# Kernel tuning notes

Hardware: AMD Instinct MI355X
Metric: run time of the kernel (lower is better)

## Reference

```python
import jax, jax.numpy as jnp
import numpy as np

B, T, C_IN, DIM, NFFT, HOP = 8, 1024, 256, 512, 1024, 256
NOUT = NFFT // 2 + 1
BB_DIL = (1, 1, 2, 2, 4, 4, 8, 8)
RES_DIL = (1, 3, 5)
N_RES = 3


def conv1d(x, w, b, dilation=1, groups=1, padding=0):
    # x: (B,C,T), w: (O, I/groups, K)
    y = jax.lax.conv_general_dilated(
        x, w, window_strides=(1,), padding=[(padding, padding)],
        rhs_dilation=(dilation,), dimension_numbers=('NCH', 'OIH', 'NCH'),
        feature_group_count=groups)
    return y + b[None, :, None]


def layernorm(x, g, b, eps=1e-6):
    m = jnp.mean(x, -1, keepdims=True)
    v = jnp.mean((x - m) ** 2, -1, keepdims=True)
    return (x - m) * jax.lax.rsqrt(v + eps) * g + b


def istft(spec, window):
    # spec: (B, F, Tf) complex, center=True, hann window, win_length=n_fft
    Bsz, F_, Tf = spec.shape
    frames = jnp.fft.irfft(spec, n=NFFT, axis=1)            # (B, n_fft, Tf)
    frames = jnp.transpose(frames, (0, 2, 1)) * window       # (B, Tf, n_fft)
    L = NFFT + HOP * (Tf - 1)
    idx = jnp.arange(Tf)[:, None] * HOP + jnp.arange(NFFT)[None, :]  # (Tf, n_fft)
    y = jnp.zeros((Bsz, L), frames.dtype).at[:, idx].add(frames)
    env = jnp.zeros((L,), window.dtype).at[idx].add(
        jnp.broadcast_to(window ** 2, (Tf, NFFT)))
    y = y / jnp.where(env > 1e-11, env, 1.0)
    start = NFFT // 2
    return y[:, start:start + HOP * (Tf - 1)]


def setup_inputs() -> dict:
    key = jax.random.key(0)
    ks = iter(jax.random.split(key, 64))
    r = lambda *s: jax.random.normal(next(ks), s, jnp.float32) * 0.02
    return {
        'x': jax.random.normal(next(ks), (B, T, C_IN), jnp.float32),
        'conv_in_w': r(DIM, C_IN, 7), 'conv_in_b': r(DIM),
        'skip_w': r(DIM, C_IN, 1), 'skip_b': r(DIM),
        'bb_dw_w': r(8, DIM, 1, 7), 'bb_dw_b': r(8, DIM),
        'bb_ln_g': jnp.ones((8, DIM), jnp.float32), 'bb_ln_b': jnp.zeros((8, DIM), jnp.float32),
        'bb_pw1_w': r(8, 4 * DIM, DIM), 'bb_pw1_b': r(8, 4 * DIM),
        'bb_pw2_w': r(8, DIM, 4 * DIM), 'bb_pw2_b': r(8, DIM),
        'bb_gamma': jnp.full((8, DIM), 1e-6, jnp.float32),
        'res_w1': r(N_RES, 3, DIM, DIM, 3), 'res_b1': r(N_RES, 3, DIM),
        'res_w2': r(N_RES, 3, DIM, DIM, 3), 'res_b2': r(N_RES, 3, DIM),
        'ln_g': jnp.ones((DIM,), jnp.float32), 'ln_b': jnp.zeros((DIM,), jnp.float32),
        'mag_w1': r(DIM, DIM), 'mag_b1': r(DIM),
        'mag_w2': r(NOUT, DIM), 'mag_b2': r(NOUT),
        'ph_w': r(NOUT, DIM), 'ph_b': r(NOUT),
        'cumsum_w': jnp.linspace(0.05, 0.4, NOUT, dtype=jnp.float32)[None, :],
        'window': (0.5 - 0.5 * jnp.cos(2.0 * jnp.pi * jnp.arange(NFFT) / NFFT)).astype(jnp.float32),
    }


def reference(x, conv_in_w, conv_in_b, skip_w, skip_b,
              bb_dw_w, bb_dw_b, bb_ln_g, bb_ln_b,
              bb_pw1_w, bb_pw1_b, bb_pw2_w, bb_pw2_b, bb_gamma,
              res_w1, res_b1, res_w2, res_b2,
              ln_g, ln_b, mag_w1, mag_b1, mag_w2, mag_b2,
              ph_w, ph_b, cumsum_w, window):
    # (B,T,C) -> (B,C,T)
    h = jnp.transpose(x, (0, 2, 1))
    skip = conv1d(h, skip_w, skip_b)                     # (B,DIM,T)
    hp = jnp.pad(h, ((0, 0), (0, 0), (3, 3)), mode='reflect')
    h = conv1d(hp, conv_in_w, conv_in_b)                 # kernel 7, pad 0 -> (B,DIM,T)
    # ConvNeXt backbone
    for i, d in enumerate(BB_DIL):
        res = h
        pad = (7 + (d - 1) * 6) // 2
        y = conv1d(h, bb_dw_w[i], bb_dw_b[i], dilation=d, groups=DIM, padding=pad)
        y = jnp.transpose(y, (0, 2, 1))                  # (B,T,DIM)
        y = layernorm(y, bb_ln_g[i], bb_ln_b[i])
        y = jax.nn.gelu(y @ bb_pw1_w[i].T + bb_pw1_b[i], approximate=False)
        y = y @ bb_pw2_w[i].T + bb_pw2_b[i]
        y = bb_gamma[i] * y
        h = res + jnp.transpose(y, (0, 2, 1))
    h = h + skip                                         # same length T
    # Residual dilated conv stacks
    for i in range(N_RES):
        for j, d in enumerate(RES_DIL):
            y = conv1d(h, res_w1[i, j], res_b1[i, j], dilation=d, padding=d)
            y = jax.nn.leaky_relu(y, 0.1)
            y = conv1d(y, res_w2[i, j], res_b2[i, j], padding=1)
            h = h + y
    h = jnp.transpose(h, (0, 2, 1))                      # (B,T,DIM)
    h = layernorm(h, ln_g, ln_b)
    # magnitude head
    m = jax.nn.gelu(h @ mag_w1.T + mag_b1, approximate=False)
    log_mag = m @ mag_w2.T + mag_b2
    mag = jnp.exp(jnp.clip(log_mag, -10.0, 10.0))        # (B,T,NOUT)
    # instantaneous-frequency phase head
    inst = jnp.tanh(h @ ph_w.T + ph_b) * jnp.pi
    phase = jnp.cumsum(inst * cumsum_w, axis=1)
    phase = jnp.remainder(phase + jnp.pi, 2.0 * jnp.pi) - jnp.pi
    # synthesize
    spec = jax.lax.complex(mag * jnp.cos(phase), mag * jnp.sin(phase))
    spec = jnp.transpose(spec, (0, 2, 1))                # (B,F,T)
    return istft(spec, window)
```

## Files before the change

kernel.cpp:

```cpp
#include <hip/hip_runtime.h>
#include <math.h>

constexpr int Bv = 8, Tv = 1024, DIMC = 512, NOUTC = 513;
constexpr int Mrows = Bv * Tv;
constexpr int LDS_S = 1056;
constexpr float PI_F = 3.14159265358979323846f;
constexpr float TWOPI_F = 6.28318530717958647692f;

struct TapInfo { int n; int off[7]; };
struct PtrTable { _Float16* h[36]; };

enum { BND_NONE = 0, BND_ZERO, BND_REFLECT };

typedef _Float16 half8v __attribute__((ext_vector_type(8)));
typedef float f32x4 __attribute__((ext_vector_type(4)));

__device__ __forceinline__ void gld_lds16(const void* g, void* l) {
  __builtin_amdgcn_global_load_lds(
      (const __attribute__((address_space(1))) unsigned int*)g,
      (__attribute__((address_space(3))) unsigned int*)l, 16, 0, 0);
}

enum { MEPI_GELU_H = 0, MEPI_GAMMARES };

template<int EPI, int TN>
__global__ __launch_bounds__(256)
void mfma_gemm(const _Float16* __restrict__ A, int lda,
               const _Float16* __restrict__ W, int K,
               const float* __restrict__ bias,
               const float* __restrict__ aux,
               float* __restrict__ hio,
               _Float16* __restrict__ Ch,
               int N, int ldc)
{
  constexpr int NFR = TN / 32;
  __shared__ _Float16 sA[2][128 * 32];
  __shared__ _Float16 sB[2][TN * 32];
  const int m0 = blockIdx.x * 128;
  const int n0 = blockIdx.y * TN;
  const int tid = threadIdx.x;
  const int wid = tid >> 6, lane = tid & 63;
  const int wr = wid >> 1, wc = wid & 1;
  const int fr = lane & 15, fq = lane >> 4;

  f32x4 acc[4][NFR] = {};

  const int rbase = tid >> 2;
  const int kwithin = (tid & 3) * 8;
  const int nkc = K >> 5;
  const int aBase = (wr * 64 + fr) * 32 + fq * 8;
  const int bBase = (wc * (TN / 2) + fr) * 32 + fq * 8;

  const _Float16* arow[2];
  #pragma unroll
  for (int s = 0; s < 2; ++s)
    arow[s] = A + (size_t)(m0 + s * 64 + rbase) * lda + kwithin;

  auto STAGE = [&](int kc, int buf) {
    const int k0 = kc << 5;
    #pragma unroll
    for (int s = 0; s < 2; ++s)
      gld_lds16(arow[s] + k0, (char*)&sA[buf][0] + s * 4096 + wid * 1024);
    #pragma unroll
    for (int s = 0; s < TN / 64; ++s) {
      size_t bo = (size_t)(n0 + s * 64 + rbase) * K + kwithin + k0;
      gld_lds16(W + bo, (char*)&sB[buf][0] + s * 4096 + wid * 1024);
    }
  };
  auto COMPUTE = [&](int buf) {
    half8v aF[4], bF[NFR];
    #pragma unroll
    for (int i = 0; i < 4; ++i) aF[i] = *(const half8v*)&sA[buf][aBase + i * 512];
    #pragma unroll
    for (int j = 0; j < NFR; ++j) bF[j] = *(const half8v*)&sB[buf][bBase + j * 512];
    #pragma unroll
    for (int i = 0; i < 4; ++i)
      #pragma unroll
      for (int j = 0; j < NFR; ++j)
        acc[i][j] = __builtin_amdgcn_mfma_f32_16x16x32_f16(aF[i], bF[j], acc[i][j], 0, 0, 0);
  };

  STAGE(0, 0);
  __syncthreads();
  int cur = 0;
  for (int kc = 0; kc < nkc; ++kc) {
    if (kc + 1 < nkc) STAGE(kc + 1, cur ^ 1);
    COMPUTE(cur);
    __syncthreads();
    cur ^= 1;
  }

  #pragma unroll
  for (int j = 0; j < NFR; ++j) {
    const int n = n0 + wc * (TN / 2) + j * 16 + fr;
    const float bj = bias[n];
    const float gj = (EPI == MEPI_GAMMARES) ? aux[n] : 0.f;
    #pragma unroll
    for (int i = 0; i < 4; ++i) {
      const int mB = m0 + wr * 64 + i * 16 + fq * 4;
      #pragma unroll
      for (int r = 0; r < 4; ++r) {
        const int m = mB + r;
        float v = acc[i][j][r] + bj;
        if (EPI == MEPI_GELU_H) {
          v = 0.5f * v * (1.f + erff(v * 0.70710678118654752f));
          Ch[(size_t)m * ldc + n] = (_Float16)v;
        } else {
          hio[(size_t)m * ldc + n] += gj * v;
        }
      }
    }
  }
}

enum { SEPI_F32 = 0, SEPI_LEAKY_SPLIT, SEPI_ADDRES_SPLIT,
       SEPI_GELU_SPLIT, SEPI_EXPCLIP, SEPI_TANHCW };

template<int EPI, int BND, int TN>
__global__ __launch_bounds__(256)
void mfma_gemm_split(const _Float16* __restrict__ Ah, const _Float16* __restrict__ Al, int lda,
                     const _Float16* __restrict__ Wh, const _Float16* __restrict__ Wl, int K,
                     const float* __restrict__ bias,
                     const float* __restrict__ aux,
                     float* __restrict__ hio,
                     float* __restrict__ Cf,
                     _Float16* __restrict__ Chh, _Float16* __restrict__ Chl,
                     int N, int ldc,
                     const _Float16* __restrict__ zpage,
                     TapInfo taps)
{
  constexpr int NFR = TN / 32;
  __shared__ _Float16 sAh[2][128 * 32];
  __shared__ _Float16 sAl[2][128 * 32];
  __shared__ _Float16 sBh[2][TN * 32];
  __shared__ _Float16 sBl[2][TN * 32];
  const int m0 = blockIdx.x * 128;
  const int n0 = blockIdx.y * TN;
  const int tid = threadIdx.x;
  const int wid = tid >> 6, lane = tid & 63;
  const int wr = wid >> 1, wc = wid & 1;
  const int fr = lane & 15, fq = lane >> 4;

  f32x4 acc[4][NFR] = {};

  const int t0 = m0 & (Tv - 1);
  const int rbase = tid >> 2;
  const int kwithin = (tid & 3) * 8;
  const int nkc = K >> 5;
  const int NT = taps.n * nkc;
  const int aBase = (wr * 64 + fr) * 32 + fq * 8;
  const int bBase = (wc * (TN / 2) + fr) * 32 + fq * 8;

  auto STAGE = [&](int st, int buf) {
    int tap = (taps.n == 1) ? 0 : (st / nkc);
    int kc = st - tap * nkc;
    const int k0 = kc << 5;
    const int off = (BND == BND_NONE) ? 0 : taps.off[tap];
    const _Float16* Wth = Wh + (size_t)tap * N * K;
    const _Float16* Wtl = Wl + (size_t)tap * N * K;
    #pragma unroll
    for (int s = 0; s < 2; ++s) {
      int t = t0 + s * 64 + rbase + off;
      bool valid = true;
      if (BND == BND_REFLECT) t = (t < 0) ? -t : (t >= Tv ? 2 * Tv - 2 - t : t);
      else if (BND == BND_ZERO) valid = (t >= 0) && (t < Tv);
      size_t ro = (size_t)(m0 - t0 + t) * lda + kwithin + k0;
      const void* sh = valid ? (const void*)(Ah + ro) : (const void*)zpage;
      const void* sl = valid ? (const void*)(Al + ro) : (const void*)zpage;
      gld_lds16(sh, (char*)&sAh[buf][0] + s * 4096 + wid * 1024);
      gld_lds16(sl, (char*)&sAl[buf][0] + s * 4096 + wid * 1024);
    }
    #pragma unroll
    for (int s = 0; s < TN / 64; ++s) {
      size_t bo = (size_t)(n0 + s * 64 + rbase) * K + kwithin + k0;
      gld_lds16(Wth + bo, (char*)&sBh[buf][0] + s * 4096 + wid * 1024);
      gld_lds16(Wtl + bo, (char*)&sBl[buf][0] + s * 4096 + wid * 1024);
    }
  };

  auto COMPUTE = [&](int buf) {
    half8v ah[4], al[4], bh[NFR], bl[NFR];
    #pragma unroll
    for (int i = 0; i < 4; ++i) {
      ah[i] = *(const half8v*)&sAh[buf][aBase + i * 512];
      al[i] = *(const half8v*)&sAl[buf][aBase + i * 512];
    }
    #pragma unroll
    for (int j = 0; j < NFR; ++j) {
      bh[j] = *(const half8v*)&sBh[buf][bBase + j * 512];
      bl[j] = *(const half8v*)&sBl[buf][bBase + j * 512];
    }
    #pragma unroll
    for (int i = 0; i < 4; ++i)
      #pragma unroll
      for (int j = 0; j < NFR; ++j) {
        acc[i][j] = __builtin_amdgcn_mfma_f32_16x16x32_f16(ah[i], bh[j], acc[i][j], 0, 0, 0);
        acc[i][j] = __builtin_amdgcn_mfma_f32_16x16x32_f16(ah[i], bl[j], acc[i][j], 0, 0, 0);
        acc[i][j] = __builtin_amdgcn_mfma_f32_16x16x32_f16(al[i], bh[j], acc[i][j], 0, 0, 0);
      }
  };

  STAGE(0, 0);
  __syncthreads();
  int cur = 0;
  for (int st = 0; st < NT; ++st) {
    if (st + 1 < NT) STAGE(st + 1, cur ^ 1);
    COMPUTE(cur);
    __syncthreads();
    cur ^= 1;
  }

  #pragma unroll
  for (int j = 0; j < NFR; ++j) {
    const int n = n0 + wc * (TN / 2) + j * 16 + fr;
    const bool nok = (n < N);
    const float bj = (nok && bias) ? bias[n] : 0.f;
    const float ax = (EPI == SEPI_TANHCW && nok) ? aux[n] : 0.f;
    #pragma unroll
    for (int i = 0; i < 4; ++i) {
      const int mB = m0 + wr * 64 + i * 16 + fq * 4;
      #pragma unroll
      for (int r = 0; r < 4; ++r) {
        const int m = mB + r;
        float v = acc[i][j][r] + bj;
        if (!nok) continue;
        if (EPI == SEPI_F32) {
          Cf[(size_t)m * ldc + n] = v;
        } else if (EPI == SEPI_GELU_SPLIT) {
          v = 0.5f * v * (1.f + erff(v * 0.70710678118654752f));
          _Float16 hi = (_Float16)v;
          Chh[(size_t)m * ldc + n] = hi;
          Chl[(size_t)m * ldc + n] = (_Float16)(v - (float)hi);
        } else if (EPI == SEPI_EXPCLIP) {
          Cf[(size_t)m * ldc + n] = expf(fminf(fmaxf(v, -10.f), 10.f));
        } else if (EPI == SEPI_TANHCW) {
          Cf[(size_t)m * ldc + n] = tanhf(v) * PI_F * ax;
        }
      }
    }
  }
}

enum { REPI_LEAKY = 0, REPI_ADDRES };

template<int EPI>
__global__ __launch_bounds__(256)
void res_gemm(const _Float16* __restrict__ Ah, const _Float16* __restrict__ Al,
              const _Float16* __restrict__ Wh, const _Float16* __restrict__ Wl,
              const float* __restrict__ bias,
              float* __restrict__ hio,
              _Float16* __restrict__ Chh, _Float16* __restrict__ Chl,
              const _Float16* __restrict__ zpage,
              int d)
{
  __shared__ _Float16 sAh_[160 * 32];
  __shared__ _Float16 sAl_[160 * 32];
  __shared__ _Float16 sB_[3 * 2 * 64 * 32];
  const int m0 = blockIdx.x * 128;
  const int n0 = blockIdx.y * 64;
  const int tid = threadIdx.x;
  const int wid = tid >> 6, lane = tid & 63;
  const int wr = wid >> 1, wc = wid & 1;
  const int fr = lane & 15, fq = lane >> 4;
  const int t0 = m0 & (Tv - 1);

  f32x4 acc[4][2] = {};
  const int offs[3] = {-d, 0, d};

  for (int kc = 0; kc < 16; ++kc) {
    const int k0h = kc << 5;
    #pragma unroll
    for (int it = 0; it < 5; ++it) {
      int cb = it * 4 + wid;
      int half = (cb >= 10) ? 1 : 0;
      int rb = (cb - half * 10) * 16;
      int row = rb + (lane >> 2);
      int slot_g = (lane & 3) ^ ((row >> 1) & 3);
      int t = t0 - 16 + row;
      bool valid = (t >= 0) && (t < Tv);
      const _Float16* srcb = half ? Al : Ah;
      const void* src = valid
          ? (const void*)(srcb + (size_t)(m0 - t0 + t) * DIMC + k0h + slot_g * 8)
          : (const void*)(zpage + slot_g * 8);
      void* dst = (char*)(half ? sAl_ : sAh_) + rb * 64;
      gld_lds16(src, dst);
    }
    #pragma unroll
    for (int it = 0; it < 6; ++it) {
      int cb = it * 4 + wid;
      int tap = cb >> 3;
      int r2 = cb & 7;
      int half = r2 >> 2;
      int rb = (r2 & 3) * 16;
      int row = rb + (lane >> 2);
      int slot_g = (lane & 3) ^ ((row >> 1) & 3);
      const _Float16* srcb = (half ? Wl : Wh) + (size_t)tap * 512 * 512
                           + (size_t)(n0 + row) * 512 + k0h + slot_g * 8;
      void* dst = (char*)sB_ + ((size_t)(tap * 2 + half) * 64 + rb) * 64;
      gld_lds16(srcb, dst);
    }
    __syncthreads();

    #pragma unroll
    for (int tap = 0; tap < 3; ++tap) {
      const int off = offs[tap];
      half8v ah[4], al[4], bh[2], bl[2];
      #pragma unroll
      for (int i = 0; i < 4; ++i) {
        int rA = wr * 64 + i * 16 + fr + off + 16;
        int ab = rA * 64 + ((fq ^ ((rA >> 1) & 3)) * 16);
        ah[i] = *(const half8v*)((const char*)sAh_ + ab);
        al[i] = *(const half8v*)((const char*)sAl_ + ab);
      }
      #pragma unroll
      for (int j = 0; j < 2; ++j) {
        int rB = wc * 32 + j * 16 + fr;
        int bb = rB * 64 + ((fq ^ ((rB >> 1) & 3)) * 16);
        bh[j] = *(const half8v*)((const char*)sB_ + (tap * 2 + 0) * 4096 + bb);
        bl[j] = *(const half8v*)((const char*)sB_ + (tap * 2 + 1) * 4096 + bb);
      }
      #pragma unroll
      for (int i = 0; i < 4; ++i)
        #pragma unroll
        for (int j = 0; j < 2; ++j) {
          acc[i][j] = __builtin_amdgcn_mfma_f32_16x16x32_f16(ah[i], bh[j], acc[i][j], 0, 0, 0);
          acc[i][j] = __builtin_amdgcn_mfma_f32_16x16x32_f16(ah[i], bl[j], acc[i][j], 0, 0, 0);
          acc[i][j] = __builtin_amdgcn_mfma_f32_16x16x32_f16(al[i], bh[j], acc[i][j], 0, 0, 0);
        }
    }
    __syncthreads();
  }

  #pragma unroll
  for (int j = 0; j < 2; ++j) {
    const int n = n0 + wc * 32 + j * 16 + fr;
    const float bj = bias[n];
    #pragma unroll
    for (int i = 0; i < 4; ++i) {
      const int mB = m0 + wr * 64 + i * 16 + fq * 4;
      #pragma unroll
      for (int r = 0; r < 4; ++r) {
        const int m = mB + r;
        float v = acc[i][j][r] + bj;
        if (EPI == REPI_LEAKY) {
          v = (v > 0.f) ? v : 0.1f * v;
          _Float16 hi = (_Float16)v;
          Chh[(size_t)m * DIMC + n] = hi;
          Chl[(size_t)m * DIMC + n] = (_Float16)(v - (float)hi);
        } else {
          float nh = hio[(size_t)m * DIMC + n] + v;
          hio[(size_t)m * DIMC + n] = nh;
          _Float16 hi = (_Float16)nh;
          Chh[(size_t)m * DIMC + n] = hi;
          Chl[(size_t)m * DIMC + n] = (_Float16)(nh - (float)hi);
        }
      }
    }
  }
}

__global__ __launch_bounds__(256)
void dwln(const float* __restrict__ h, const float* __restrict__ w,
          const float* __restrict__ bias, const float* __restrict__ g,
          const float* __restrict__ be, _Float16* __restrict__ out, int d)
{
  int wid = threadIdx.x >> 6, lane = threadIdx.x & 63;
  int m = (blockIdx.x << 2) + wid;
  int t = m & (Tv - 1);
  int bT = m - t;
  float acc[8];
  #pragma unroll
  for (int q = 0; q < 8; ++q) {
    int c = lane + (q << 6);
    float s = bias[c];
    #pragma unroll
    for (int k = 0; k < 7; ++k) {
      int tt = t + (k - 3) * d;
      if (tt >= 0 && tt < Tv) s = fmaf(h[(size_t)(bT + tt) * DIMC + c], w[c * 7 + k], s);
    }
    acc[q] = s;
  }
  float sum = 0.f;
  #pragma unroll
  for (int q = 0; q < 8; ++q) sum += acc[q];
  #pragma unroll
  for (int o = 32; o > 0; o >>= 1) sum += __shfl_xor(sum, o);
  float mean = sum * (1.f / 512.f);
  float vs = 0.f;
  #pragma unroll
  for (int q = 0; q < 8; ++q) { float dd = acc[q] - mean; vs = fmaf(dd, dd, vs); }
  #pragma unroll
  for (int o = 32; o > 0; o >>= 1) vs += __shfl_xor(vs, o);
  float rstd = rsqrtf(vs * (1.f / 512.f) + 1e-6f);
  #pragma unroll
  for (int q = 0; q < 8; ++q) {
    int c = lane + (q << 6);
    out[(size_t)m * DIMC + c] = (_Float16)((acc[q] - mean) * rstd * g[c] + be[c]);
  }
}

__global__ __launch_bounds__(256)
void lnorm_split(const float* __restrict__ in, const float* __restrict__ g,
                 const float* __restrict__ be,
                 _Float16* __restrict__ ohi, _Float16* __restrict__ olo)
{
  int wid = threadIdx.x >> 6, lane = threadIdx.x & 63;
  int m = (blockIdx.x << 2) + wid;
  const float* row = in + (size_t)m * DIMC;
  float acc[8];
  #pragma unroll
  for (int q = 0; q < 8; ++q) acc[q] = row[lane + (q << 6)];
  float sum = 0.f;
  #pragma unroll
  for (int q = 0; q < 8; ++q) sum += acc[q];
  #pragma unroll
  for (int o = 32; o > 0; o >>= 1) sum += __shfl_xor(sum, o);
  float mean = sum * (1.f / 512.f);
  float vs = 0.f;
  #pragma unroll
  for (int q = 0; q < 8; ++q) { float dd = acc[q] - mean; vs = fmaf(dd, dd, vs); }
  #pragma unroll
  for (int o = 32; o > 0; o >>= 1) vs += __shfl_xor(vs, o);
  float rstd = rsqrtf(vs * (1.f / 512.f) + 1e-6f);
  #pragma unroll
  for (int q = 0; q < 8; ++q) {
    int c = lane + (q << 6);
    float v = (acc[q] - mean) * rstd * g[c] + be[c];
    _Float16 hi = (_Float16)v;
    ohi[(size_t)m * DIMC + c] = hi;
    olo[(size_t)m * DIMC + c] = (_Float16)(v - (float)hi);
  }
}

__global__ __launch_bounds__(256)
void add_split(float* __restrict__ a, const float* __restrict__ b,
               _Float16* __restrict__ hi, _Float16* __restrict__ lo, int n)
{
  int i = blockIdx.x * 256 + threadIdx.x;
  if (i < n) {
    float v = a[i] + b[i]; a[i] = v;
    _Float16 h = (_Float16)v;
    hi[i] = h; lo[i] = (_Float16)(v - (float)h);
  }
}

__global__ __launch_bounds__(256)
void cvt_split(const float* __restrict__ in, _Float16* __restrict__ hi,
               _Float16* __restrict__ lo, int n)
{
  int i = blockIdx.x * 256 + threadIdx.x;
  if (i < n) {
    float v = in[i];
    _Float16 h = (_Float16)v;
    hi[i] = h; lo[i] = (_Float16)(v - (float)h);
  }
}

__global__ __launch_bounds__(256)
void cvt_split_pad(const float* __restrict__ in, _Float16* __restrict__ hi,
                   _Float16* __restrict__ lo, int rows, int cols, int padRows)
{
  int i = blockIdx.x * 256 + threadIdx.x;
  if (i >= padRows * cols) return;
  int r = i / cols;
  float v = (r < rows) ? in[i] : 0.f;
  _Float16 h = (_Float16)v;
  hi[i] = h; lo[i] = (_Float16)(v - (float)h);
}

__global__ __launch_bounds__(256)
void cvt_h(const float* __restrict__ in, _Float16* __restrict__ out, int n)
{
  int i = (blockIdx.x * 256 + threadIdx.x) * 4;
  if (i >= n) return;
  float4 v = *(const float4*)&in[i];
  out[i + 0] = (_Float16)v.x; out[i + 1] = (_Float16)v.y;
  out[i + 2] = (_Float16)v.z; out[i + 3] = (_Float16)v.w;
}

__global__ __launch_bounds__(256)
void repack_split(const float* __restrict__ in, _Float16* __restrict__ hi,
                  _Float16* __restrict__ lo, int O, int C, int KT)
{
  int idx = blockIdx.x * 256 + threadIdx.x;
  if (idx >= O * C) return;
  int o = idx / C, c = idx - o * C;
  for (int k = 0; k < KT; ++k) {
    float v = in[((size_t)o * C + c) * KT + k];
    _Float16 h = (_Float16)v;
    size_t dst = ((size_t)k * O + o) * C + c;
    hi[dst] = h; lo[dst] = (_Float16)(v - (float)h);
  }
}

__global__ __launch_bounds__(256)
void repack_all(const float* __restrict__ res_w1, const float* __restrict__ res_w2,
                PtrTable pt)
{
  int blk = blockIdx.x;
  int conv = blk >> 10;
  int idx = ((blk & 1023) << 8) + threadIdx.x;
  int o = idx >> 9, c = idx & 511;
  const float* src = (conv < 9) ? (res_w1 + (size_t)conv * 786432)
                                : (res_w2 + (size_t)(conv - 9) * 786432);
  _Float16* hi = pt.h[conv * 2];
  _Float16* lo = pt.h[conv * 2 + 1];
  #pragma unroll
  for (int k = 0; k < 3; ++k) {
    float v = src[((size_t)o * 512 + c) * 3 + k];
    _Float16 hh = (_Float16)v;
    size_t dst = ((size_t)k * 512 + o) * 512 + c;
    hi[dst] = hh; lo[dst] = (_Float16)(v - (float)hh);
  }
}

__global__ __launch_bounds__(256)
void zero_fill16(_Float16* __restrict__ p)
{
  int i = threadIdx.x * 8;
  #pragma unroll
  for (int q = 0; q < 8; ++q) p[i + q] = (_Float16)0.f;
}

__global__ __launch_bounds__(256)
void build_basis_split(const float* __restrict__ window,
                       _Float16* __restrict__ bhi, _Float16* __restrict__ blo)
{
  int n = blockIdx.x;
  float wn = window[n];
  const float invN = 1.f / 1024.f;
  for (int j = threadIdx.x; j < LDS_S; j += 256) {
    float coef = 0.f;
    if (j < 513) {
      int k = j;
      if (k == 0)        coef = invN;
      else if (k == 512) coef = (n & 1) ? -invN : invN;
      else {
        int r = (k * n) & 1023;
        coef = 2.f * invN * cosf(TWOPI_F * (float)r * (1.f / 1024.f));
      }
    } else if (j < 1026) {
      int k = j - 513;
      if (k != 0 && k != 512) {
        int r = (k * n) & 1023;
        coef = -2.f * invN * sinf(TWOPI_F * (float)r * (1.f / 1024.f));
      }
    }
    float v = coef * wn;
    _Float16 hi = (_Float16)v;
    bhi[(size_t)n * LDS_S + j] = hi;
    blo[(size_t)n * LDS_S + j] = (_Float16)(v - (float)hi);
  }
}

__global__ __launch_bounds__(256)
void scan_part(const float* __restrict__ dph, float* __restrict__ psum)
{
  int b = blockIdx.x, fg = blockIdx.y;
  int w = threadIdx.x >> 6, lane = threadIdx.x & 63;
  int tc = blockIdx.z * 4 + w;
  int f = fg * 64 + lane;
  if (f >= NOUTC) return;
  const float* p = dph + (size_t)(b * Tv + tc * 32) * NOUTC + f;
  float s = 0.f;
  #pragma unroll 8
  for (int j = 0; j < 32; ++j) s += p[(size_t)j * NOUTC];
  psum[((size_t)b * 32 + tc) * 520 + f] = s;
}

__global__ __launch_bounds__(256)
void scan_off(float* __restrict__ psum)
{
  int idx = blockIdx.x * 256 + threadIdx.x;
  if (idx >= 8 * NOUTC) return;
  int b = idx / NOUTC, f = idx - b * NOUTC;
  float run = 0.f;
  for (int tc = 0; tc < 32; ++tc) {
    size_t o = ((size_t)b * 32 + tc) * 520 + f;
    float v = psum[o];
    psum[o] = run;
    run += v;
  }
}

__global__ __launch_bounds__(256)
void scan_emit(const float* __restrict__ dph, const float* __restrict__ mag,
               const float* __restrict__ psum,
               _Float16* __restrict__ Shi, _Float16* __restrict__ Slo)
{
  int b = blockIdx.x, fg = blockIdx.y;
  int w = threadIdx.x >> 6, lane = threadIdx.x & 63;
  int tc = blockIdx.z * 4 + w;
  int f = fg * 64 + lane;
  if (f >= NOUTC) return;
  float run = psum[((size_t)b * 32 + tc) * 520 + f];
  const size_t base = (size_t)(b * Tv + tc * 32) * NOUTC + f;
  for (int j = 0; j < 32; ++j) {
    run += dph[base + (size_t)j * NOUTC];
    float r = fmodf(run + PI_F, TWOPI_F);
    if (r < 0.f) r += TWOPI_F;
    float wph = r - PI_F;
    float mg = mag[base + (size_t)j * NOUTC];
    float sn, cs;
    sincosf(wph, &sn, &cs);
    size_t mrow = (size_t)(b * Tv + tc * 32 + j) * LDS_S;
    float vc = mg * cs, vs2 = mg * sn;
    _Float16 hc = (_Float16)vc, hs = (_Float16)vs2;
    Shi[mrow + f] = hc;        Slo[mrow + f] = (_Float16)(vc - (float)hc);
    Shi[mrow + 513 + f] = hs;  Slo[mrow + 513 + f] = (_Float16)(vs2 - (float)hs);
  }
}

__global__ __launch_bounds__(256)
void pad_S(_Float16* __restrict__ Shi, _Float16* __restrict__ Slo)
{
  int idx = blockIdx.x * 256 + threadIdx.x;
  if (idx >= Mrows * 30) return;
  int m = idx / 30, c = 1026 + idx % 30;
  Shi[(size_t)m * LDS_S + c] = (_Float16)0.f;
  Slo[(size_t)m * LDS_S + c] = (_Float16)0.f;
}

__global__ __launch_bounds__(256)
void ola(const float* __restrict__ frames, const float* __restrict__ window,
         float* __restrict__ out)
{
  int idx = blockIdx.x * 256 + threadIdx.x;
  if (idx >= Bv * 261888) return;
  int b = idx / 261888;
  int i = idx - b * 261888;
  int l = i + 512;
  int tmax = l >> 8; if (tmax > 1023) tmax = 1023;
  int tmin = (l >= 1023) ? ((l - 1023 + 255) >> 8) : 0;
  float acc = 0.f, env = 0.f;
  for (int t = tmin; t <= tmax; ++t) {
    int n = l - (t << 8);
    acc += frames[(size_t)(b * Tv + t) * 1024 + n];
    float wv = window[n];
    env = fmaf(wv, wv, env);
  }
  out[idx] = acc / (env > 1e-11f ? env : 1.f);
}

extern "C" void kernel_launch(void* const* d_in, const int* in_sizes, int n_in,
                              void* d_out, int out_size, void* d_ws, size_t ws_size,
                              hipStream_t stream)
{
  const float* x         = (const float*)d_in[0];
  const float* conv_in_w = (const float*)d_in[1];
  const float* conv_in_b = (const float*)d_in[2];
  const float* skip_w    = (const float*)d_in[3];
  const float* skip_b    = (const float*)d_in[4];
  const float* bb_dw_w   = (const float*)d_in[5];
  const float* bb_dw_b   = (const float*)d_in[6];
  const float* bb_ln_g   = (const float*)d_in[7];
  const float* bb_ln_b   = (const float*)d_in[8];
  const float* bb_pw1_w  = (const float*)d_in[9];
  const float* bb_pw1_b  = (const float*)d_in[10];
  const float* bb_pw2_w  = (const float*)d_in[11];
  const float* bb_pw2_b  = (const float*)d_in[12];
  const float* bb_gamma  = (const float*)d_in[13];
  const float* res_w1    = (const float*)d_in[14];
  const float* res_b1    = (const float*)d_in[15];
  const float* res_w2    = (const float*)d_in[16];
  const float* res_b2    = (const float*)d_in[17];
  const float* ln_g      = (const float*)d_in[18];
  const float* ln_b      = (const float*)d_in[19];
  const float* mag_w1    = (const float*)d_in[20];
  const float* mag_b1    = (const float*)d_in[21];
  const float* mag_w2    = (const float*)d_in[22];
  const float* mag_b2    = (const float*)d_in[23];
  const float* ph_w      = (const float*)d_in[24];
  const float* ph_b      = (const float*)d_in[25];
  const float* cumsum_w  = (const float*)d_in[26];
  const float* window    = (const float*)d_in[27];
  float* out = (float*)d_out;
  float* ws  = (float*)d_ws;

  float* w_h     = ws;
  float* w_skip  = ws + 4194304;
  float* w_t4    = ws + 8388608;
  float* w_mag   = ws + 12582912;
  float* w_dph   = ws + 16785408;
  float* w_basis = ws + 20987904;
  float* w_big   = ws + 22069248;
  _Float16* t3h  = (_Float16*)w_big;
  _Float16* h_hi = (_Float16*)w_big;
  _Float16* h_lo = h_hi + 4194304;
  _Float16* y_hi = h_hi + 8388608;
  _Float16* y_lo = h_hi + 12582912;
  _Float16* Shi  = (_Float16*)w_big;
  _Float16* Slo  = Shi + 8650752;
  float* w_frames= w_h;

  _Float16* t2h  = (_Float16*)(ws + 30720000);
  _Float16* x_hi = (_Float16*)(ws + 32817152);
  _Float16* x_lo = (_Float16*)(ws + 33865728);
  _Float16* wA_hi= (_Float16*)(ws + 34914304);
  _Float16* wA_lo= (_Float16*)(ws + 35438592);
  _Float16* wB_hi= (_Float16*)(ws + 35962880);
  _Float16* wB_lo= (_Float16*)(ws + 36487168);
  _Float16* zpg  = (_Float16*)(ws + 37011456);
  float* w_psum  = ws + 37012480;

  _Float16* wpw1h = (_Float16*)w_t4;
  _Float16* wpw2h = (_Float16*)w_mag;

  static const size_t slotOffF[18] = {
    8388608, 9175040, 9961472, 10747904, 11534336,
    12582912, 13369344, 14155776, 14942208, 15728640,
    16785408, 17571840, 18358272, 19144704, 19931136,
    32817152, 33603584,
    30720000
  };
  PtrTable pt;
  for (int cv = 0; cv < 18; ++cv) {
    _Float16* hi = (_Float16*)(ws + slotOffF[cv]);
    pt.h[cv * 2] = hi;
    pt.h[cv * 2 + 1] = hi + 786432;
  }

  _Float16* lshi = (_Float16*)w_skip;
  _Float16* lslo = lshi + 4194304;
  _Float16* t4hi = (_Float16*)w_t4;
  _Float16* t4lo = t4hi + 4194304;
  _Float16* m1hi = t2h;
  _Float16* m1lo = t2h + 262144;
  _Float16* m2hi = t2h + 524288;
  _Float16* m2lo = t2h + 851968;
  _Float16* phhi = t2h + 1179648;
  _Float16* phlo = t2h + 1507328;
  _Float16* bhi  = (_Float16*)w_basis;
  _Float16* blo  = bhi + 1081344;

  dim3 blk(256);
  TapInfo tp1{1, {0}};

  zero_fill16<<<dim3(1), blk, 0, stream>>>(zpg);
  cvt_split<<<dim3(8192 * 256 / 256), blk, 0, stream>>>(x, x_hi, x_lo, 8192 * 256);
  cvt_h<<<dim3(8388608 / 4 / 256), blk, 0, stream>>>(bb_pw1_w, wpw1h, 8388608);
  cvt_h<<<dim3(8388608 / 4 / 256), blk, 0, stream>>>(bb_pw2_w, wpw2h, 8388608);

  repack_split<<<dim3(512 * 256 / 256), blk, 0, stream>>>(conv_in_w, wA_hi, wA_lo, 512, 256, 7);
  {
    TapInfo tp{7, {-3, -2, -1, 0, 1, 2, 3}};
    mfma_gemm_split<SEPI_F32, BND_REFLECT, 64><<<dim3(64, 8), blk, 0, stream>>>(
        x_hi, x_lo, 256, wA_hi, wA_lo, 256, conv_in_b, nullptr, nullptr, w_h, nullptr, nullptr,
        512, 512, zpg, tp);
  }
  repack_split<<<dim3(512 * 256 / 256), blk, 0, stream>>>(skip_w, wB_hi, wB_lo, 512, 256, 1);
  mfma_gemm_split<SEPI_F32, BND_NONE, 64><<<dim3(64, 8), blk, 0, stream>>>(
      x_hi, x_lo, 256, wB_hi, wB_lo, 256, skip_b, nullptr, nullptr, w_skip, nullptr, nullptr,
      512, 512, zpg, tp1);

  const int dil[8] = {1, 1, 2, 2, 4, 4, 8, 8};
  for (int i = 0; i < 8; ++i) {
    dwln<<<dim3(2048), blk, 0, stream>>>(w_h, bb_dw_w + i * 512 * 7, bb_dw_b + i * 512,
                                         bb_ln_g + i * 512, bb_ln_b + i * 512, t2h, dil[i]);
    mfma_gemm<MEPI_GELU_H, 128><<<dim3(64, 16), blk, 0, stream>>>(
        t2h, 512, wpw1h + (size_t)i * 2048 * 512, 512, bb_pw1_b + i * 2048,
        nullptr, nullptr, t3h, 2048, 2048);
    mfma_gemm<MEPI_GAMMARES, 64><<<dim3(64, 8), blk, 0, stream>>>(
        t3h, 2048, wpw2h + (size_t)i * 512 * 2048, 2048, bb_pw2_b + i * 512,
        bb_gamma + i * 512, w_h, nullptr, 512, 512);
  }
  add_split<<<dim3(4194304 / 256), blk, 0, stream>>>(w_h, w_skip, h_hi, h_lo, 4194304);

  repack_all<<<dim3(18 * 1024), blk, 0, stream>>>(res_w1, res_w2, pt);

  const int rdil[3] = {1, 3, 5};
  for (int i = 0; i < 3; ++i)
    for (int j = 0; j < 3; ++j) {
      int d = rdil[j];
      int idx = i * 3 + j;
      res_gemm<REPI_LEAKY><<<dim3(64, 8), blk, 0, stream>>>(
          h_hi, h_lo, pt.h[idx * 2], pt.h[idx * 2 + 1],
          res_b1 + idx * 512, nullptr, y_hi, y_lo, zpg, d);
      res_gemm<REPI_ADDRES><<<dim3(64, 8), blk, 0, stream>>>(
          y_hi, y_lo, pt.h[(9 + idx) * 2], pt.h[(9 + idx) * 2 + 1],
          res_b2 + idx * 512, w_h, h_hi, h_lo, zpg, 1);
    }

  lnorm_split<<<dim3(2048), blk, 0, stream>>>(w_h, ln_g, ln_b, lshi, lslo);

  cvt_split<<<dim3(262144 / 256), blk, 0, stream>>>(mag_w1, m1hi, m1lo, 262144);
  cvt_split_pad<<<dim3(640 * 512 / 256), blk, 0, stream>>>(mag_w2, m2hi, m2lo, 513, 512, 640);
  cvt_split_pad<<<dim3(640 * 512 / 256), blk, 0, stream>>>(ph_w, phhi, phlo, 513, 512, 640);

  mfma_gemm_split<SEPI_GELU_SPLIT, BND_NONE, 64><<<dim3(64, 8), blk, 0, stream>>>(
      lshi, lslo, 512, m1hi, m1lo, 512, mag_b1, nullptr, nullptr, nullptr,
      t4hi, t4lo, 512, 512, zpg, tp1);
  mfma_gemm_split<SEPI_EXPCLIP, BND_NONE, 64><<<dim3(64, 10), blk, 0, stream>>>(
      t4hi, t4lo, 512, m2hi, m2lo, 512, mag_b2, nullptr, nullptr, w_mag,
      nullptr, nullptr, 513, 513, zpg, tp1);
  mfma_gemm_split<SEPI_TANHCW, BND_NONE, 64><<<dim3(64, 10), blk, 0, stream>>>(
      lshi, lslo, 512, phhi, phlo, 512, ph_b, cumsum_w, nullptr, w_dph,
      nullptr, nullptr, 513, 513, zpg, tp1);

  build_basis_split<<<dim3(1024), blk, 0, stream>>>(window, bhi, blo);
  pad_S<<<dim3((Mrows * 30 + 255) / 256), blk, 0, stream>>>(Shi, Slo);
  scan_part<<<dim3(8, 9, 8), blk, 0, stream>>>(w_dph, w_psum);
  scan_off<<<dim3(17), blk, 0, stream>>>(w_psum);
  scan_emit<<<dim3(8, 9, 8), blk, 0, stream>>>(w_dph, w_mag, w_psum, Shi, Slo);
  mfma_gemm_split<SEPI_F32, BND_NONE, 64><<<dim3(64, 16), blk, 0, stream>>>(
      Shi, Slo, LDS_S, bhi, blo, LDS_S, nullptr, nullptr, nullptr, w_frames,
      nullptr, nullptr, 1024, 1024, zpg, tp1);
  ola<<<dim3((Bv * 261888 + 255) / 256), blk, 0, stream>>>(w_frames, window, out);
}
```

Before: 2.015 ms.

## Swizzle GEMM LDS layout, vectorize split/convert kernels, widen iSTFT GEMM tile

Applies an XOR swizzle to the k-chunk position when staging A/B tiles into LDS, with matching swizzled fragment reads, so that MFMA fragment loads from shared memory hit fewer bank conflicts. Element-wise split and convert kernels now process four floats per thread with vector loads and stores, and their launch grids are adjusted to match. The frame-synthesis GEMM uses a 128-wide N tile with half the blocks, which doubles LDS use per block and may lower occupancy.

Measured after the change: 1.976 ms. Within noise of the previous version (-1.9%).

```diff
diff --git a/kernel.cpp b/kernel.cpp
--- a/kernel.cpp
+++ b/kernel.cpp
@@ -2,7 +2,7 @@
 #include <math.h>
 
 constexpr int Bv = 8, Tv = 1024, DIMC = 512, NOUTC = 513;
-constexpr int Mrows = Bv * Tv;
+constexpr int Mrows = Bv * 1024;
 constexpr int LDS_S = 1056;
 constexpr float PI_F = 3.14159265358979323846f;
 constexpr float TWOPI_F = 6.28318530717958647692f;
@@ -13,6 +13,7 @@
 enum { BND_NONE = 0, BND_ZERO, BND_REFLECT };
 
 typedef _Float16 half8v __attribute__((ext_vector_type(8)));
+typedef _Float16 half4v __attribute__((ext_vector_type(4)));
 typedef float f32x4 __attribute__((ext_vector_type(4)));
 
 __device__ __forceinline__ void gld_lds16(const void* g, void* l) {
@@ -46,15 +47,16 @@
   f32x4 acc[4][NFR] = {};
 
   const int rbase = tid >> 2;
-  const int kwithin = (tid & 3) * 8;
+  const int kwS = (((tid & 3) ^ ((tid >> 3) & 3)) << 3);
   const int nkc = K >> 5;
-  const int aBase = (wr * 64 + fr) * 32 + fq * 8;
-  const int bBase = (wc * (TN / 2) + fr) * 32 + fq * 8;
+  const int fqS = fq ^ ((fr >> 1) & 3);
+  const int aBase = (wr * 64 + fr) * 32 + fqS * 8;
+  const int bBase = (wc * (TN / 2) + fr) * 32 + fqS * 8;
 
   const _Float16* arow[2];
   #pragma unroll
   for (int s = 0; s < 2; ++s)
-    arow[s] = A + (size_t)(m0 + s * 64 + rbase) * lda + kwithin;
+    arow[s] = A + (size_t)(m0 + s * 64 + rbase) * lda + kwS;
 
   auto STAGE = [&](int kc, int buf) {
     const int k0 = kc << 5;
@@ -63,7 +65,7 @@
       gld_lds16(arow[s] + k0, (char*)&sA[buf][0] + s * 4096 + wid * 1024);
     #pragma unroll
     for (int s = 0; s < TN / 64; ++s) {
-      size_t bo = (size_t)(n0 + s * 64 + rbase) * K + kwithin + k0;
+      size_t bo = (size_t)(n0 + s * 64 + rbase) * K + kwS + k0;
       gld_lds16(W + bo, (char*)&sB[buf][0] + s * 4096 + wid * 1024);
     }
   };
@@ -145,11 +147,12 @@
 
   const int t0 = m0 & (Tv - 1);
   const int rbase = tid >> 2;
-  const int kwithin = (tid & 3) * 8;
+  const int kwS = (((tid & 3) ^ ((tid >> 3) & 3)) << 3);
   const int nkc = K >> 5;
   const int NT = taps.n * nkc;
-  const int aBase = (wr * 64 + fr) * 32 + fq * 8;
-  const int bBase = (wc * (TN / 2) + fr) * 32 + fq * 8;
+  const int fqS = fq ^ ((fr >> 1) & 3);
+  const int aBase = (wr * 64 + fr) * 32 + fqS * 8;
+  const int bBase = (wc * (TN / 2) + fr) * 32 + fqS * 8;
 
   auto STAGE = [&](int st, int buf) {
     int tap = (taps.n == 1) ? 0 : (st / nkc);
@@ -164,7 +167,7 @@
       bool valid = true;
       if (BND == BND_REFLECT) t = (t < 0) ? -t : (t >= Tv ? 2 * Tv - 2 - t : t);
       else if (BND == BND_ZERO) valid = (t >= 0) && (t < Tv);
-      size_t ro = (size_t)(m0 - t0 + t) * lda + kwithin + k0;
+      size_t ro = (size_t)(m0 - t0 + t) * lda + kwS + k0;
       const void* sh = valid ? (const void*)(Ah + ro) : (const void*)zpage;
       const void* sl = valid ? (const void*)(Al + ro) : (const void*)zpage;
       gld_lds16(sh, (char*)&sAh[buf][0] + s * 4096 + wid * 1024);
@@ -172,7 +175,7 @@
     }
     #pragma unroll
     for (int s = 0; s < TN / 64; ++s) {
-      size_t bo = (size_t)(n0 + s * 64 + rbase) * K + kwithin + k0;
+      size_t bo = (size_t)(n0 + s * 64 + rbase) * K + kwS + k0;
       gld_lds16(Wth + bo, (char*)&sBh[buf][0] + s * 4096 + wid * 1024);
       gld_lds16(Wtl + bo, (char*)&sBl[buf][0] + s * 4096 + wid * 1024);
     }
@@ -436,24 +439,38 @@
 void add_split(float* __restrict__ a, const float* __restrict__ b,
                _Float16* __restrict__ hi, _Float16* __restrict__ lo, int n)
 {
-  int i = blockIdx.x * 256 + threadIdx.x;
-  if (i < n) {
-    float v = a[i] + b[i]; a[i] = v;
-    _Float16 h = (_Float16)v;
-    hi[i] = h; lo[i] = (_Float16)(v - (float)h);
-  }
+  int i = (blockIdx.x * 256 + threadIdx.x) * 4;
+  if (i >= n) return;
+  float4 va = *(const float4*)&a[i];
+  float4 vb = *(const float4*)&b[i];
+  float v[4] = {va.x + vb.x, va.y + vb.y, va.z + vb.z, va.w + vb.w};
+  *(float4*)&a[i] = make_float4(v[0], v[1], v[2], v[3]);
+  half4v h, l;
+  #pragma unroll
+  for (int q = 0; q < 4; ++q) {
+    _Float16 hh = (_Float16)v[q];
+    h[q] = hh; l[q] = (_Float16)(v[q] - (float)hh);
+  }
+  *(half4v*)&hi[i] = h;
+  *(half4v*)&lo[i] = l;
 }
 
 __global__ __launch_bounds__(256)
 void cvt_split(const float* __restrict__ in, _Float16* __restrict__ hi,
                _Float16* __restrict__ lo, int n)
 {
-  int i = blockIdx.x * 256 + threadIdx.x;
-  if (i < n) {
-    float v = in[i];
-    _Float16 h = (_Float16)v;
-    hi[i] = h; lo[i] = (_Float16)(v - (float)h);
-  }
+  int i = (blockIdx.x * 256 + threadIdx.x) * 4;
+  if (i >= n) return;
+  float4 vv = *(const float4*)&in[i];
+  float v[4] = {vv.x, vv.y, vv.z, vv.w};
+  half4v h, l;
+  #pragma unroll
+  for (int q = 0; q < 4; ++q) {
+    _Float16 hh = (_Float16)v[q];
+    h[q] = hh; l[q] = (_Float16)(v[q] - (float)hh);
+  }
+  *(half4v*)&hi[i] = h;
+  *(half4v*)&lo[i] = l;
 }
 
 __global__ __launch_bounds__(256)
@@ -474,8 +491,10 @@
   int i = (blockIdx.x * 256 + threadIdx.x) * 4;
   if (i >= n) return;
   float4 v = *(const float4*)&in[i];
-  out[i + 0] = (_Float16)v.x; out[i + 1] = (_Float16)v.y;
-  out[i + 2] = (_Float16)v.z; out[i + 3] = (_Float16)v.w;
+  half4v h;
+  h[0] = (_Float16)v.x; h[1] = (_Float16)v.y;
+  h[2] = (_Float16)v.z; h[3] = (_Float16)v.w;
+  *(half4v*)&out[i] = h;
 }
 
 __global__ __launch_bounds__(256)
@@ -737,7 +756,7 @@
   TapInfo tp1{1, {0}};
 
   zero_fill16<<<dim3(1), blk, 0, stream>>>(zpg);
-  cvt_split<<<dim3(8192 * 256 / 256), blk, 0, stream>>>(x, x_hi, x_lo, 8192 * 256);
+  cvt_split<<<dim3(8192 * 256 / 4 / 256), blk, 0, stream>>>(x, x_hi, x_lo, 8192 * 256);
   cvt_h<<<dim3(8388608 / 4 / 256), blk, 0, stream>>>(bb_pw1_w, wpw1h, 8388608);
   cvt_h<<<dim3(8388608 / 4 / 256), blk, 0, stream>>>(bb_pw2_w, wpw2h, 8388608);
 
@@ -764,7 +783,7 @@
         t3h, 2048, wpw2h + (size_t)i * 512 * 2048, 2048, bb_pw2_b + i * 512,
         bb_gamma + i * 512, w_h, nullptr, 512, 512);
   }
-  add_split<<<dim3(4194304 / 256), blk, 0, stream>>>(w_h, w_skip, h_hi, h_lo, 4194304);
+  add_split<<<dim3(4194304 / 4 / 256), blk, 0, stream>>>(w_h, w_skip, h_hi, h_lo, 4194304);
 
   repack_all<<<dim3(18 * 1024), blk, 0, stream>>>(res_w1, res_w2, pt);
 
@@ -783,7 +802,7 @@
 
   lnorm_split<<<dim3(2048), blk, 0, stream>>>(w_h, ln_g, ln_b, lshi, lslo);
 
-  cvt_split<<<dim3(262144 / 256), blk, 0, stream>>>(mag_w1, m1hi, m1lo, 262144);
+  cvt_split<<<dim3(262144 / 4 / 256), blk, 0, stream>>>(mag_w1, m1hi, m1lo, 262144);
   cvt_split_pad<<<dim3(640 * 512 / 256), blk, 0, stream>>>(mag_w2, m2hi, m2lo, 513, 512, 640);
   cvt_split_pad<<<dim3(640 * 512 / 256), blk, 0, stream>>>(ph_w, phhi, phlo, 513, 512, 640);
 
@@ -802,7 +821,7 @@
   scan_part<<<dim3(8, 9, 8), blk, 0, stream>>>(w_dph, w_psum);
   scan_off<<<dim3(17), blk, 0, stream>>>(w_psum);
   scan_emit<<<dim3(8, 9, 8), blk, 0, stream>>>(w_dph, w_mag, w_psum, Shi, Slo);
-  mfma_gemm_split<SEPI_F32, BND_NONE, 64><<<dim3(64, 16), blk, 0, stream>>>(
+  mfma_gemm_split<SEPI_F32, BND_NONE, 128><<<dim3(64, 8), blk, 0, stream>>>(
       Shi, Slo, LDS_S, bhi, blo, LDS_S, nullptr, nullptr, nullptr, w_frames,
       nullptr, nullptr, 1024, 1024, zpg, tp1);
   ola<<<dim3((Bv * 261888 + 255) / 256), blk, 0, stream>>>(w_frames, window, out);
```
